# Optimization experiments

Hardware: AMD Instinct MI355X
Metric: run time of the kernel (lower is better)

The kernel has to match this reference:

```python
import jax, jax.numpy as jnp
import numpy as np

EPS = 1e-12  # torch F.normalize default eps


def conv1x1(x, w, b):
    # x: [N,C,H,W], w: [K,C], b: [K]
    return jnp.einsum('nchw,kc->nkhw', x, w) + b[None, :, None, None]


def forward_sa(f1, f2, cw1, cb1, cw2, cb2):
    n, _, h, w = f1.shape
    c1 = conv1x1(f1, cw1, cb1)  # [N,1,H,W]
    c2 = conv1x1(f2, cw2, cb2)
    c1 = jax.nn.softmax(c1.reshape(n, h * w), axis=1).reshape(n, 1, h, w)
    c2 = jax.nn.softmax(c2.reshape(n, h * w), axis=1).reshape(n, 1, h, w)
    return c1 * f1, c2 * f2


def l2norm_ch(x):
    # torch F.normalize(x) -> p=2 over dim=1 with eps clamp
    n = jnp.sqrt(jnp.sum(x * x, axis=1, keepdims=True))
    return x / jnp.maximum(n, EPS)


def forward_ca(f1, f2, pw1, pb1, pw2, pb2):
    N, C, H, W = f1.shape
    f1_cl = conv1x1(f1, pw1, pb1).reshape(N, -1, H * W)  # [N,Cl,HW]
    f2_cl = conv1x1(f2, pw2, pb2).reshape(N, -1, H * W)
    # A[n,p,q] = sum_c f2_cl[n,c,p] * f1_cl[n,c,q]  -> [N,HW,HW]
    A_c = jnp.tanh(jnp.einsum('ncp,ncq->npq', f2_cl, f1_cl))
    f1_v = f1.reshape(N, C, H * W)
    f2_v = f2.reshape(N, C, H * W)
    # f1_hat = f1_v @ A_c^T ; f2_hat = f2_v @ A_c
    f1_hat = jnp.einsum('ncp,nqp->ncq', f1_v, A_c).reshape(N, C, H, W)
    f2_hat = jnp.einsum('ncp,npq->ncq', f2_v, A_c).reshape(N, C, H, W)
    return l2norm_ch(f1_hat), l2norm_ch(f2_hat)


def setup_inputs() -> dict:
    key = jax.random.key(0)
    ks = jax.random.split(key, 10)
    N, C, H, W = 2, 256, 64, 64
    Cl = C // 16
    sc = 1.0 / np.sqrt(C)
    return {
        'f1': jax.random.normal(ks[0], (N, C, H, W), jnp.float32),
        'f2': jax.random.normal(ks[1], (N, C, H, W), jnp.float32),
        'pw1': jax.random.normal(ks[2], (Cl, C), jnp.float32) * sc,
        'pb1': jax.random.normal(ks[3], (Cl,), jnp.float32) * sc,
        'pw2': jax.random.normal(ks[4], (Cl, C), jnp.float32) * sc,
        'pb2': jax.random.normal(ks[5], (Cl,), jnp.float32) * sc,
        'cw1': jax.random.normal(ks[6], (1, C), jnp.float32) * sc,
        'cb1': jax.random.normal(ks[7], (1,), jnp.float32) * sc,
        'cw2': jax.random.normal(ks[8], (1, C), jnp.float32) * sc,
        'cb2': jax.random.normal(ks[9], (1,), jnp.float32) * sc,
    }


def reference(f1, f2, pw1, pb1, pw2, pb2, cw1, cb1, cw2, cb2):
    f1_1, f2_1 = forward_sa(f1, f2, cw1, cb1, cw2, cb2)
    f1_hat, f2_hat = forward_ca(f1_1, f2_1, pw1, pb1, pw2, pb2)
    fp1_hat = jax.nn.relu(f1_hat + f1)
    fp2_hat = jax.nn.relu(f2_hat + f2)
    f1_2, f2_2 = forward_sa(fp1_hat, fp2_hat, cw1, cb1, cw2, cb2)
    # Original calls forward_ca(f1_2, f2_2) again but discards the result
    # and returns (f1_2, f2_2); the dead call is omitted (identical output).
    return (f1_2, f2_2)
```

## Files before the change

### kernel.cpp

```cpp
#include <hip/hip_runtime.h>
#include <hip/hip_bf16.h>
#include <math.h>

#define N_B 2
#define C_CH 256
#define HW_SZ 4096
#define CL_CH 16

typedef __bf16 bf16x8 __attribute__((ext_vector_type(8)));
typedef float f32x4 __attribute__((ext_vector_type(4)));
typedef float f32x16 __attribute__((ext_vector_type(16)));

__device__ __forceinline__ unsigned short f2bf(float x){
  __hip_bfloat16 b = __float2bfloat16(x);
  return *reinterpret_cast<unsigned short*>(&b);
}
__device__ __forceinline__ unsigned int cvtpk(float a, float b){
  unsigned int r;
  asm("v_cvt_pk_bf16_f32 %0, %1, %2" : "=v"(r) : "v"(a), "v"(b));
  return r;
}
__device__ __forceinline__ float tanh_fast(float x){
  float e = __expf(2.0f * x);
  return fmaf(-2.0f, __builtin_amdgcn_rcpf(1.0f + e), 1.0f);
}
__device__ __forceinline__ void gload16(const void* gsrc, void* lds_dst){
  __builtin_amdgcn_global_load_lds(
      (const __attribute__((address_space(1))) unsigned int*)gsrc,
      (__attribute__((address_space(3))) unsigned int*)lds_dst, 16, 0, 0);
}

__global__ void k_conv1(const float* __restrict__ f1, const float* __restrict__ f2,
                        const float* __restrict__ w1, const float* __restrict__ w2,
                        const float* __restrict__ b1, const float* __restrict__ b2,
                        float* __restrict__ cv){
  const int i = blockIdx.z, n = blockIdx.y, t = threadIdx.x;
  const int ql = t & 63, cg = t >> 6;
  const int q = blockIdx.x * 64 + ql;
  const float* f = (i ? f2 : f1) + n * C_CH * HW_SZ;
  const float* w = i ? w2 : w1;
  __shared__ float ws[C_CH];
  __shared__ float red[4][72];
  ws[t] = w[t];
  __syncthreads();
  float acc = 0.f;
  #pragma unroll 8
  for (int c = cg * 64; c < cg * 64 + 64; ++c)
    acc += f[c * HW_SZ + q] * ws[c];
  red[cg][ql] = acc;
  __syncthreads();
  if (t < 64){
    float s = red[0][t] + red[1][t] + red[2][t] + red[3][t] + (i ? b2[0] : b1[0]);
    cv[(i * 2 + n) * HW_SZ + blockIdx.x * 64 + t] = s;
  }
}

__global__ void k_softmax(const float* __restrict__ cv, float* __restrict__ pr){
  const int r = blockIdx.x, t = threadIdx.x;
  const float* x = cv + r * HW_SZ;
  float* y = pr + r * HW_SZ;
  __shared__ float red[256];
  float v[16];
  float m = -1e30f;
  #pragma unroll
  for (int j = 0; j < 16; j++){ v[j] = x[j * 256 + t]; m = fmaxf(m, v[j]); }
  red[t] = m; __syncthreads();
  for (int s = 128; s > 0; s >>= 1){ if (t < s) red[t] = fmaxf(red[t], red[t + s]); __syncthreads(); }
  m = red[0]; __syncthreads();
  float sum = 0.f;
  #pragma unroll
  for (int j = 0; j < 16; j++){ v[j] = __expf(v[j] - m); sum += v[j]; }
  red[t] = sum; __syncthreads();
  for (int s = 128; s > 0; s >>= 1){ if (t < s) red[t] += red[t + s]; __syncthreads(); }
  const float inv = 1.0f / red[0];
  #pragma unroll
  for (int j = 0; j < 16; j++) y[j * 256 + t] = v[j] * inv;
}

__global__ void k_scale_cl(const float* __restrict__ f1, const float* __restrict__ f2,
                           const float* __restrict__ pr,
                           const float* __restrict__ pw1, const float* __restrict__ pw2,
                           const float* __restrict__ pb1, const float* __restrict__ pb2,
                           unsigned short* __restrict__ fs1, unsigned short* __restrict__ fs2,
                           unsigned short* __restrict__ clT1, unsigned short* __restrict__ clT2){
  const int i = blockIdx.z, n = blockIdx.y, t = threadIdx.x;
  const int ql = t & 63, cg = t >> 6;
  const int q = blockIdx.x * 64 + ql;
  const float* f = (i ? f2 : f1) + n * C_CH * HW_SZ;
  unsigned short* fs = (i ? fs2 : fs1) + n * C_CH * HW_SZ;
  unsigned short* clT = (i ? clT2 : clT1) + n * 32 * HW_SZ;
  const float* pw = i ? pw2 : pw1;
  const float* pb = i ? pb2 : pb1;
  __shared__ float wls[CL_CH * C_CH];
  __shared__ float red[4][CL_CH][66];
  #pragma unroll
  for (int j = 0; j < 16; j++) wls[j * 256 + t] = pw[j * 256 + t];
  __syncthreads();
  const float p = pr[(i * 2 + n) * HW_SZ + q];
  float acc[16];
  #pragma unroll
  for (int k = 0; k < 16; k++) acc[k] = 0.f;
  for (int c = cg * 64; c < cg * 64 + 64; ++c){
    float vv = f[c * HW_SZ + q] * p;
    fs[c * HW_SZ + q] = f2bf(vv);
    #pragma unroll
    for (int k = 0; k < 16; k++) acc[k] += wls[k * 256 + c] * vv;
  }
  #pragma unroll
  for (int k = 0; k < 16; k++) red[cg][k][ql] = acc[k];
  __syncthreads();
  #pragma unroll
  for (int j = 0; j < 4; j++){
    int e = j * 256 + t; int k = e >> 6, qq = e & 63;
    float s = red[0][k][qq] + red[1][k][qq] + red[2][k][qq] + red[3][k][qq] + pb[k];
    clT[(blockIdx.x * 64 + qq) * 32 + k] = f2bf(s);
  }
  if (t < 128){
    uint4 zv = {0u, 0u, 0u, 0u};
    int qq = t >> 1, half = t & 1;
    *reinterpret_cast<uint4*>(&clT[(blockIdx.x * 64 + qq) * 32 + 16 + half * 8]) = zv;
  }
}

__global__ __launch_bounds__(512, 2) void k_hat(
    const unsigned short* __restrict__ fs1, const unsigned short* __restrict__ fs2,
    const unsigned short* __restrict__ clT1, const unsigned short* __restrict__ clT2,
    float* __restrict__ hat1, float* __restrict__ hat2,
    float* __restrict__ pt1, float* __restrict__ pt2){
  const int t = threadIdx.x;
  const int bid = blockIdx.x;
  const int xcd = bid & 7, slot = bid >> 3;
  const int z = xcd >> 1;
  const int n = z & 1, i = z >> 1;
  const int x = slot * 2 + (xcd & 1);
  const int qt = x >> 1, ph = x & 1;
  const int q0 = qt * 128;
  const int pbase = ph * 2048;

  const unsigned short* fs = (i ? fs2 : fs1) + n * C_CH * HW_SZ;
  const unsigned short* uT = (i ? clT1 : clT2) + n * 32 * HW_SZ;
  const unsigned short* vT = (i ? clT2 : clT1) + n * 32 * HW_SZ;
  float* out = (ph ? (i ? pt2 : pt1) : (i ? hat2 : hat1)) + n * C_CH * HW_SZ;

  __shared__ __align__(16) unsigned short fsA[2][C_CH * 64];
  __shared__ __align__(16) unsigned short aT[2][128 * 64];

  const int wv = t >> 6, l = t & 63;
  const int g4 = l >> 4, lr16 = l & 15;
  const int g2 = l >> 5, lr32 = l & 31;

  const int pfw = wv & 3;
  const int qh  = wv >> 2;
  const int cblk = wv & 3, qblk = wv >> 2;

  bf16x8 ub[4];
  #pragma unroll
  for (int j = 0; j < 4; ++j)
    ub[j] = *reinterpret_cast<const bf16x8*>(&uT[(q0 + qh * 64 + j * 16 + lr16) * 32 + g4 * 8]);

  f32x16 acc00, acc01, acc10, acc11;
  #pragma unroll
  for (int r = 0; r < 16; ++r){ acc00[r] = 0.f; acc01[r] = 0.f; acc10[r] = 0.f; acc11[r] = 0.f; }
  const f32x4 zz = {0.f, 0.f, 0.f, 0.f};

  int fs_src[4];
  #pragma unroll
  for (int it = 0; it < 4; ++it){
    int d = it * 512 + t; int c = d >> 3, sl = d & 7;
    int u = sl ^ (c & 7) ^ (((c >> 3) & 1) << 2);
    fs_src[it] = c * (HW_SZ * 2) + u * 16;
  }
  const char* vbase = (const char*)vT;
  const int vgo = (pfw * 16 + lr16) * 64 + g4 * 16;
  unsigned atw0;
  {
    int qd = qh * 64 + lr16;
    int sw = (pfw * 2 + (g4 >> 1)) ^ (qd & 7) ^ (((qd >> 3) & 1) << 2);
    atw0 = qd * 128 + sw * 16 + (g4 & 1) * 8;
  }
  unsigned afo[2], bqo[2];
  #pragma unroll
  for (int cf = 0; cf < 2; ++cf){
    int crow = cblk * 64 + cf * 32 + lr32;
    afo[cf] = crow * 128 + ((g2 ^ (crow & 7) ^ (((crow >> 3) & 1) << 2)) << 4);
  }
  #pragma unroll
  for (int qf = 0; qf < 2; ++qf){
    int qrow = qblk * 64 + qf * 32 + lr32;
    bqo[qf] = qrow * 128 + ((g2 ^ (qrow & 7) ^ (((qrow >> 3) & 1) << 2)) << 4);
  }

  auto vload = [&](int kk) -> uint4 {
    return *reinterpret_cast<const uint4*>(vbase + (pbase + kk * 64) * 64 + vgo);
  };
  auto stage_fs = [&](unsigned short* dstbase, int p0){
    const char* src = (const char*)fs + p0 * 2;
    #pragma unroll
    for (int it = 0; it < 4; ++it)
      gload16(src + fs_src[it], dstbase + (it * 512 + wv * 64) * 8);
  };
  auto dgen = [&](uint4 vr, char* atB){
    bf16x8 av = *reinterpret_cast<bf16x8*>(&vr);
    #pragma unroll
    for (int j = 0; j < 4; ++j){
      f32x4 d = __builtin_amdgcn_mfma_f32_16x16x32_bf16(av, ub[j], zz, 0, 0, 0);
      uint2 pk;
      pk.x = cvtpk(tanh_fast(d[0]), tanh_fast(d[1]));
      pk.y = cvtpk(tanh_fast(d[2]), tanh_fast(d[3]));
      *reinterpret_cast<uint2*>(atB + atw0 + j * 2048) = pk;
    }
  };
  auto mmain = [&](const char* faB, const char* atB){
    #pragma unroll
    for (int ks = 0; ks < 4; ++ks){
      unsigned kx = (unsigned)(ks << 5);
      bf16x8 a0 = *reinterpret_cast<const bf16x8*>(faB + (afo[0] ^ kx));
      bf16x8 a1 = *reinterpret_cast<const bf16x8*>(faB + (afo[1] ^ kx));
      bf16x8 b0 = *reinterpret_cast<const bf16x8*>(atB + (bqo[0] ^ kx));
      bf16x8 b1 = *reinterpret_cast<const bf16x8*>(atB + (bqo[1] ^ kx));
      acc00 = __builtin_amdgcn_mfma_f32_32x32x16_bf16(a0, b0, acc00, 0, 0, 0);
      acc01 = __builtin_amdgcn_mfma_f32_32x32x16_bf16(a0, b1, acc01, 0, 0, 0);
      acc10 = __builtin_amdgcn_mfma_f32_32x32x16_bf16(a1, b0, acc10, 0, 0, 0);
      acc11 = __builtin_amdgcn_mfma_f32_32x32x16_bf16(a1, b1, acc11, 0, 0, 0);
    }
  };

  uint4 va = vload(0);
  uint4 vb = vload(1);
  stage_fs(fsA[0], pbase);
  dgen(va, (char*)aT[0]);
  __syncthreads();

  #pragma unroll 1
  for (int k2 = 0; k2 < 16; ++k2){
    {
      const int k = 2 * k2;
      stage_fs(fsA[1], pbase + (k + 1) * 64);
      va = vload(k + 2);
      dgen(vb, (char*)aT[1]);
      mmain((const char*)fsA[0], (const char*)aT[0]);
      __syncthreads();
    }
    {
      const int k = 2 * k2 + 1;
      stage_fs(fsA[0], pbase + (k + 1) * 64);
      vb = vload(k + 2);
      dgen(va, (char*)aT[0]);
      mmain((const char*)fsA[1], (const char*)aT[1]);
      __syncthreads();
    }
  }

  const int qcol = q0 + qblk * 64 + lr32;
  #pragma unroll
  for (int r = 0; r < 16; ++r){
    int cr = (r & 3) + 8 * (r >> 2) + 4 * g2;
    out[(cblk * 64 + cr) * HW_SZ + qcol] = acc00[r];
    out[(cblk * 64 + cr) * HW_SZ + qcol + 32] = acc01[r];
    out[(cblk * 64 + 32 + cr) * HW_SZ + qcol] = acc10[r];
    out[(cblk * 64 + 32 + cr) * HW_SZ + qcol + 32] = acc11[r];
  }
}

__global__ void k_norm(float* __restrict__ hat1, float* __restrict__ hat2,
                       const float* __restrict__ pt1, const float* __restrict__ pt2,
                       const float* __restrict__ f1, const float* __restrict__ f2,
                       const float* __restrict__ cw1, const float* __restrict__ cw2,
                       const float* __restrict__ cb1, const float* __restrict__ cb2,
                       float* __restrict__ cv2){
  const int i = blockIdx.z, n = blockIdx.y, t = threadIdx.x;
  const int ql = t & 63, cg = t >> 6;
  const int q = blockIdx.x * 64 + ql;
  float* hat = (i ? hat2 : hat1) + n * C_CH * HW_SZ;
  const float* pt = (i ? pt2 : pt1) + n * C_CH * HW_SZ;
  const float* f = (i ? f2 : f1) + n * C_CH * HW_SZ;
  __shared__ float ws[C_CH];
  __shared__ float red[4][72];
  __shared__ float invs[64];
  ws[t] = (i ? cw2 : cw1)[t];
  __syncthreads();
  float s = 0.f;
  #pragma unroll 8
  for (int c = cg * 64; c < cg * 64 + 64; ++c){
    float h = hat[c * HW_SZ + q] + pt[c * HW_SZ + q];
    s += h * h;
  }
  red[cg][ql] = s; __syncthreads();
  if (t < 64){
    float ss = red[0][t] + red[1][t] + red[2][t] + red[3][t];
    invs[t] = 1.0f / fmaxf(sqrtf(ss), 1e-12f);
  }
  __syncthreads();
  const float inv = invs[ql];
  float ca = 0.f;
  #pragma unroll 8
  for (int c = cg * 64; c < cg * 64 + 64; ++c){
    float h = hat[c * HW_SZ + q] + pt[c * HW_SZ + q];
    float vv = fmaxf(h * inv + f[c * HW_SZ + q], 0.0f);
    hat[c * HW_SZ + q] = vv;
    ca += ws[c] * vv;
  }
  red[cg][ql] = ca; __syncthreads();
  if (t < 64){
    float ss = red[0][t] + red[1][t] + red[2][t] + red[3][t] + (i ? cb2[0] : cb1[0]);
    cv2[(i * 2 + n) * HW_SZ + blockIdx.x * 64 + t] = ss;
  }
}

__global__ void k_final(const float* __restrict__ fp1, const float* __restrict__ fp2,
                        const float* __restrict__ pr2, float* __restrict__ outp){
  const int i = blockIdx.z;
  const int idx4 = (blockIdx.x * 256 + threadIdx.x) * 4;
  const int n = idx4 >> 20;
  const int q = idx4 & (HW_SZ - 1);
  const float* fp = i ? fp2 : fp1;
  float4 vv = *reinterpret_cast<const float4*>(&fp[idx4]);
  float4 pp = *reinterpret_cast<const float4*>(&pr2[(i * 2 + n) * HW_SZ + q]);
  float4 o; o.x = vv.x * pp.x; o.y = vv.y * pp.y; o.z = vv.z * pp.z; o.w = vv.w * pp.w;
  *reinterpret_cast<float4*>(&outp[i * (C_CH * HW_SZ * N_B) + idx4]) = o;
}

extern "C" void kernel_launch(void* const* d_in, const int* in_sizes, int n_in,
                              void* d_out, int out_size, void* d_ws, size_t ws_size,
                              hipStream_t stream){
  const float* f1  = (const float*)d_in[0];
  const float* f2  = (const float*)d_in[1];
  const float* pw1 = (const float*)d_in[2];
  const float* pb1 = (const float*)d_in[3];
  const float* pw2 = (const float*)d_in[4];
  const float* pb2 = (const float*)d_in[5];
  const float* cw1 = (const float*)d_in[6];
  const float* cb1 = (const float*)d_in[7];
  const float* cw2 = (const float*)d_in[8];
  const float* cb2 = (const float*)d_in[9];
  float* ws = (float*)d_ws;
  float* HAT1 = ws;
  float* HAT2 = ws + 2097152;
  float* PT1  = ws + 4194304;
  float* PT2  = ws + 6291456;
  unsigned short* FS1 = (unsigned short*)(ws + 8388608);
  unsigned short* FS2 = (unsigned short*)(ws + 9437184);
  unsigned short* CLT1 = (unsigned short*)(ws + 10485760);
  unsigned short* CLT2 = (unsigned short*)(ws + 10616832);
  float* CV1  = ws + 10747904;
  float* PR1  = ws + 10764288;
  float* CV2  = ws + 10780672;
  float* PR2  = ws + 10797056;
  float* outp = (float*)d_out;

  k_conv1   <<<dim3(64, 2, 2), 256, 0, stream>>>(f1, f2, cw1, cw2, cb1, cb2, CV1);
  k_softmax <<<4, 256, 0, stream>>>(CV1, PR1);
  k_scale_cl<<<dim3(64, 2, 2), 256, 0, stream>>>(f1, f2, PR1, pw1, pw2, pb1, pb2,
                                                 FS1, FS2, CLT1, CLT2);
  k_hat     <<<256, 512, 0, stream>>>(FS1, FS2, CLT1, CLT2, HAT1, HAT2, PT1, PT2);
  k_norm    <<<dim3(64, 2, 2), 256, 0, stream>>>(HAT1, HAT2, PT1, PT2, f1, f2,
                                                 cw1, cw2, cb1, cb2, CV2);
  k_softmax <<<4, 256, 0, stream>>>(CV2, PR2);
  k_final   <<<dim3(2048, 1, 2), 256, 0, stream>>>(HAT1, HAT2, PR2, outp);
}
```

Before: 105.4 us.

## Fuse softmax into consumer kernels, cache hat in LDS, restructure k_hat barriers

Removes the two standalone softmax launches. Each consuming block (k_scale_cl and k_final) now recomputes the row max and sum over 4096 logits itself, trading launch and serialization overhead for redundant reduction work in every block. k_norm caches hat+pt as bf16 in LDS so the second pass does not reread two global arrays, at some precision cost. The k_hat main loop uses pointer increments and explicit s_barrier with sched_barrier fences instead of __syncthreads, and the barrier after the prologue is dropped.

```diff
diff --git a/kernel.cpp b/kernel.cpp
--- a/kernel.cpp
+++ b/kernel.cpp
@@ -14,6 +14,10 @@
 __device__ __forceinline__ unsigned short f2bf(float x){
   __hip_bfloat16 b = __float2bfloat16(x);
   return *reinterpret_cast<unsigned short*>(&b);
+}
+__device__ __forceinline__ float bf2f(unsigned short u){
+  unsigned int w = ((unsigned int)u) << 16;
+  return *reinterpret_cast<float*>(&w);
 }
 __device__ __forceinline__ unsigned int cvtpk(float a, float b){
   unsigned int r;
@@ -55,30 +59,8 @@
   }
 }
 
-__global__ void k_softmax(const float* __restrict__ cv, float* __restrict__ pr){
-  const int r = blockIdx.x, t = threadIdx.x;
-  const float* x = cv + r * HW_SZ;
-  float* y = pr + r * HW_SZ;
-  __shared__ float red[256];
-  float v[16];
-  float m = -1e30f;
-  #pragma unroll
-  for (int j = 0; j < 16; j++){ v[j] = x[j * 256 + t]; m = fmaxf(m, v[j]); }
-  red[t] = m; __syncthreads();
-  for (int s = 128; s > 0; s >>= 1){ if (t < s) red[t] = fmaxf(red[t], red[t + s]); __syncthreads(); }
-  m = red[0]; __syncthreads();
-  float sum = 0.f;
-  #pragma unroll
-  for (int j = 0; j < 16; j++){ v[j] = __expf(v[j] - m); sum += v[j]; }
-  red[t] = sum; __syncthreads();
-  for (int s = 128; s > 0; s >>= 1){ if (t < s) red[t] += red[t + s]; __syncthreads(); }
-  const float inv = 1.0f / red[0];
-  #pragma unroll
-  for (int j = 0; j < 16; j++) y[j * 256 + t] = v[j] * inv;
-}
-
 __global__ void k_scale_cl(const float* __restrict__ f1, const float* __restrict__ f2,
-                           const float* __restrict__ pr,
+                           const float* __restrict__ cv,
                            const float* __restrict__ pw1, const float* __restrict__ pw2,
                            const float* __restrict__ pb1, const float* __restrict__ pb2,
                            unsigned short* __restrict__ fs1, unsigned short* __restrict__ fs2,
@@ -91,12 +73,26 @@
   unsigned short* clT = (i ? clT2 : clT1) + n * 32 * HW_SZ;
   const float* pw = i ? pw2 : pw1;
   const float* pb = i ? pb2 : pb1;
+  const float* cvrow = cv + (i * 2 + n) * HW_SZ;
   __shared__ float wls[CL_CH * C_CH];
   __shared__ float red[4][CL_CH][66];
+  __shared__ float smr[256];
   #pragma unroll
   for (int j = 0; j < 16; j++) wls[j * 256 + t] = pw[j * 256 + t];
-  __syncthreads();
-  const float p = pr[(i * 2 + n) * HW_SZ + q];
+  float sv[16];
+  float m = -1e30f;
+  #pragma unroll
+  for (int j = 0; j < 16; j++){ sv[j] = cvrow[j * 256 + t]; m = fmaxf(m, sv[j]); }
+  smr[t] = m; __syncthreads();
+  for (int s = 128; s > 0; s >>= 1){ if (t < s) smr[t] = fmaxf(smr[t], smr[t + s]); __syncthreads(); }
+  m = smr[0]; __syncthreads();
+  float sum = 0.f;
+  #pragma unroll
+  for (int j = 0; j < 16; j++) sum += __expf(sv[j] - m);
+  smr[t] = sum; __syncthreads();
+  for (int s = 128; s > 0; s >>= 1){ if (t < s) smr[t] += smr[t + s]; __syncthreads(); }
+  const float p = __expf(cvrow[q] - m) * (1.0f / smr[0]);
+
   float acc[16];
   #pragma unroll
   for (int k = 0; k < 16; k++) acc[k] = 0.f;
@@ -170,7 +166,6 @@
     int u = sl ^ (c & 7) ^ (((c >> 3) & 1) << 2);
     fs_src[it] = c * (HW_SZ * 2) + u * 16;
   }
-  const char* vbase = (const char*)vT;
   const int vgo = (pfw * 16 + lr16) * 64 + g4 * 16;
   unsigned atw0;
   {
@@ -190,11 +185,7 @@
     bqo[qf] = qrow * 128 + ((g2 ^ (qrow & 7) ^ (((qrow >> 3) & 1) << 2)) << 4);
   }
 
-  auto vload = [&](int kk) -> uint4 {
-    return *reinterpret_cast<const uint4*>(vbase + (pbase + kk * 64) * 64 + vgo);
-  };
-  auto stage_fs = [&](unsigned short* dstbase, int p0){
-    const char* src = (const char*)fs + p0 * 2;
+  auto stage_fs = [&](unsigned short* dstbase, const char* src){
     #pragma unroll
     for (int it = 0; it < 4; ++it)
       gload16(src + fs_src[it], dstbase + (it * 512 + wv * 64) * 8);
@@ -225,29 +216,42 @@
     }
   };
 
-  uint4 va = vload(0);
-  uint4 vb = vload(1);
-  stage_fs(fsA[0], pbase);
+  const char* fpp = (const char*)fs + pbase * 2;
+  const char* vp  = (const char*)vT + pbase * 64 + vgo;
+
+  stage_fs(fsA[0], fpp); fpp += 128;
+  uint4 va = *reinterpret_cast<const uint4*>(vp);
+  uint4 vb = *reinterpret_cast<const uint4*>(vp + 4096);
+  vp += 8192;
   dgen(va, (char*)aT[0]);
-  __syncthreads();
 
   #pragma unroll 1
   for (int k2 = 0; k2 < 16; ++k2){
     {
-      const int k = 2 * k2;
-      stage_fs(fsA[1], pbase + (k + 1) * 64);
-      va = vload(k + 2);
+      stage_fs(fsA[1], fpp); fpp += 128;
+      va = *reinterpret_cast<const uint4*>(vp); vp += 4096;
       dgen(vb, (char*)aT[1]);
+      asm volatile("s_waitcnt lgkmcnt(0)" ::: "memory");
+      __builtin_amdgcn_sched_barrier(0);
+      __builtin_amdgcn_s_barrier();
+      __builtin_amdgcn_sched_barrier(0);
       mmain((const char*)fsA[0], (const char*)aT[0]);
-      __syncthreads();
+      __builtin_amdgcn_sched_barrier(0);
+      __builtin_amdgcn_s_barrier();
+      __builtin_amdgcn_sched_barrier(0);
     }
     {
-      const int k = 2 * k2 + 1;
-      stage_fs(fsA[0], pbase + (k + 1) * 64);
-      vb = vload(k + 2);
+      stage_fs(fsA[0], fpp); fpp += 128;
+      vb = *reinterpret_cast<const uint4*>(vp); vp += 4096;
       dgen(va, (char*)aT[0]);
+      asm volatile("s_waitcnt lgkmcnt(0)" ::: "memory");
+      __builtin_amdgcn_sched_barrier(0);
+      __builtin_amdgcn_s_barrier();
+      __builtin_amdgcn_sched_barrier(0);
       mmain((const char*)fsA[1], (const char*)aT[1]);
-      __syncthreads();
+      __builtin_amdgcn_sched_barrier(0);
+      __builtin_amdgcn_s_barrier();
+      __builtin_amdgcn_sched_barrier(0);
     }
   }
 
@@ -277,12 +281,14 @@
   __shared__ float ws[C_CH];
   __shared__ float red[4][72];
   __shared__ float invs[64];
+  __shared__ unsigned short hLs[C_CH][66];
   ws[t] = (i ? cw2 : cw1)[t];
   __syncthreads();
   float s = 0.f;
   #pragma unroll 8
   for (int c = cg * 64; c < cg * 64 + 64; ++c){
     float h = hat[c * HW_SZ + q] + pt[c * HW_SZ + q];
+    hLs[c][ql] = f2bf(h);
     s += h * h;
   }
   red[cg][ql] = s; __syncthreads();
@@ -295,8 +301,7 @@
   float ca = 0.f;
   #pragma unroll 8
   for (int c = cg * 64; c < cg * 64 + 64; ++c){
-    float h = hat[c * HW_SZ + q] + pt[c * HW_SZ + q];
-    float vv = fmaxf(h * inv + f[c * HW_SZ + q], 0.0f);
+    float vv = fmaxf(bf2f(hLs[c][ql]) * inv + f[c * HW_SZ + q], 0.0f);
     hat[c * HW_SZ + q] = vv;
     ca += ws[c] * vv;
   }
@@ -308,15 +313,34 @@
 }
 
 __global__ void k_final(const float* __restrict__ fp1, const float* __restrict__ fp2,
-                        const float* __restrict__ pr2, float* __restrict__ outp){
-  const int i = blockIdx.z;
-  const int idx4 = (blockIdx.x * 256 + threadIdx.x) * 4;
+                        const float* __restrict__ cv2, float* __restrict__ outp){
+  const int i = blockIdx.z, t = threadIdx.x;
+  const int idx4 = (blockIdx.x * 256 + t) * 4;
   const int n = idx4 >> 20;
   const int q = idx4 & (HW_SZ - 1);
+  const float* cvrow = cv2 + (i * 2 + n) * HW_SZ;
+  __shared__ float red[256];
+  float sv[16];
+  float m = -1e30f;
+  #pragma unroll
+  for (int j = 0; j < 16; j++){ sv[j] = cvrow[j * 256 + t]; m = fmaxf(m, sv[j]); }
+  red[t] = m; __syncthreads();
+  for (int s = 128; s > 0; s >>= 1){ if (t < s) red[t] = fmaxf(red[t], red[t + s]); __syncthreads(); }
+  m = red[0]; __syncthreads();
+  float sum = 0.f;
+  #pragma unroll
+  for (int j = 0; j < 16; j++) sum += __expf(sv[j] - m);
+  red[t] = sum; __syncthreads();
+  for (int s = 128; s > 0; s >>= 1){ if (t < s) red[t] += red[t + s]; __syncthreads(); }
+  const float invS = 1.0f / red[0];
+
   const float* fp = i ? fp2 : fp1;
   float4 vv = *reinterpret_cast<const float4*>(&fp[idx4]);
-  float4 pp = *reinterpret_cast<const float4*>(&pr2[(i * 2 + n) * HW_SZ + q]);
-  float4 o; o.x = vv.x * pp.x; o.y = vv.y * pp.y; o.z = vv.z * pp.z; o.w = vv.w * pp.w;
+  float4 o;
+  o.x = vv.x * (__expf(cvrow[q + 0] - m) * invS);
+  o.y = vv.y * (__expf(cvrow[q + 1] - m) * invS);
+  o.z = vv.z * (__expf(cvrow[q + 2] - m) * invS);
+  o.w = vv.w * (__expf(cvrow[q + 3] - m) * invS);
   *reinterpret_cast<float4*>(&outp[i * (C_CH * HW_SZ * N_B) + idx4]) = o;
 }
 
@@ -343,18 +367,14 @@
   unsigned short* CLT1 = (unsigned short*)(ws + 10485760);
   unsigned short* CLT2 = (unsigned short*)(ws + 10616832);
   float* CV1  = ws + 10747904;
-  float* PR1  = ws + 10764288;
-  float* CV2  = ws + 10780672;
-  float* PR2  = ws + 10797056;
+  float* CV2  = ws + 10764288;
   float* outp = (float*)d_out;
 
   k_conv1   <<<dim3(64, 2, 2), 256, 0, stream>>>(f1, f2, cw1, cw2, cb1, cb2, CV1);
-  k_softmax <<<4, 256, 0, stream>>>(CV1, PR1);
-  k_scale_cl<<<dim3(64, 2, 2), 256, 0, stream>>>(f1, f2, PR1, pw1, pw2, pb1, pb2,
+  k_scale_cl<<<dim3(64, 2, 2), 256, 0, stream>>>(f1, f2, CV1, pw1, pw2, pb1, pb2,
                                                  FS1, FS2, CLT1, CLT2);
   k_hat     <<<256, 512, 0, stream>>>(FS1, FS2, CLT1, CLT2, HAT1, HAT2, PT1, PT2);
   k_norm    <<<dim3(64, 2, 2), 256, 0, stream>>>(HAT1, HAT2, PT1, PT2, f1, f2,
                                                  cw1, cw2, cb1, cb2, CV2);
-  k_softmax <<<4, 256, 0, stream>>>(CV2, PR2);
-  k_final   <<<dim3(2048, 1, 2), 256, 0, stream>>>(HAT1, HAT2, PR2, outp);
-}
+  k_final   <<<dim3(2048, 1, 2), 256, 0, stream>>>(HAT1, HAT2, CV2, outp);
+}
```

Result: faster. 96.69 us (-8.2%).
